# Performance work log

Hardware: AMD Instinct MI355X
Metric: run time of the kernel (lower is better)

Reference implementation:

```python
import jax, jax.numpy as jnp
import numpy as np

BLOCK = 64      # BigBird block size
HEADS = 8
N_GLOBAL = 1
WINDOW = 1      # +/-1 block sliding window
N_RAND = 3


def _build_block_idx(n_blocks, seed=0):
    """Per query block: global + window + random key blocks, causal, deduped, -1 padded."""
    rng = np.random.RandomState(seed)
    m = N_GLOBAL + (2 * WINDOW + 1) + N_RAND  # 7
    idx = np.full((n_blocks, m), -1, np.int32)
    for i in range(n_blocks):
        s = set(range(min(N_GLOBAL, i + 1)))
        for w in range(i - WINDOW, i + 1):  # causal window (blocks <= i)
            if w >= 0:
                s.add(w)
        cand = [c for c in range(i + 1) if c not in s]
        rng.shuffle(cand)
        s.update(cand[:N_RAND])
        ss = sorted(s)
        idx[i, :len(ss)] = ss
    return idx


def setup_inputs() -> dict:
    key = jax.random.key(0)
    ks = jax.random.split(key, 12)
    b, S, D = 4, 4096, 768
    dff = 4 * D
    init = lambda k, shape: (0.02 * jax.random.normal(k, shape, jnp.float32))
    return {
        'q': jax.random.normal(ks[0], (b, S, D), jnp.float32),
        'ln1_g': jnp.ones((D,), jnp.float32), 'ln1_b': jnp.zeros((D,), jnp.float32),
        'Wq': init(ks[1], (D, D)), 'bq': jnp.zeros((D,), jnp.float32),
        'Wk': init(ks[2], (D, D)), 'bk': jnp.zeros((D,), jnp.float32),
        'Wv': init(ks[3], (D, D)), 'bv': jnp.zeros((D,), jnp.float32),
        'Wo': init(ks[4], (D, D)), 'bo': jnp.zeros((D,), jnp.float32),
        'ln2_g': jnp.ones((D,), jnp.float32), 'ln2_b': jnp.zeros((D,), jnp.float32),
        'W1': init(ks[5], (D, dff)), 'b1': jnp.zeros((dff,), jnp.float32),
        'W2': init(ks[6], (dff, D)), 'b2': jnp.zeros((D,), jnp.float32),
        'key_block_idx': jnp.asarray(_build_block_idx(S // BLOCK), jnp.int32),
    }


def _layernorm(x, g, b, eps=1e-5):
    mu = jnp.mean(x, axis=-1, keepdims=True)
    var = jnp.mean(jnp.square(x - mu), axis=-1, keepdims=True)
    return (x - mu) * jax.lax.rsqrt(var + eps) * g + b


def _bigbird_attn(x, Wq, bq, Wk, bk, Wv, bv, Wo, bo, key_block_idx):
    b, S, D = x.shape
    H, hd = HEADS, D // HEADS
    nb = S // BLOCK
    m = key_block_idx.shape[1]
    proj = lambda W, bias: (x @ W + bias).reshape(b, nb, BLOCK, H, hd).transpose(0, 3, 1, 2, 4)
    q = proj(Wq, bq)  # [b,h,nb,B,hd]
    k = proj(Wk, bk)
    v = proj(Wv, bv)
    valid = key_block_idx >= 0                      # [nb, m]
    idx = jnp.maximum(key_block_idx, 0)
    kg = k[:, :, idx]                               # [b,h,nb,m,B,hd]
    vg = v[:, :, idx]
    scores = jnp.einsum('bhnqd,bhnmkd->bhnqmk', q, kg) / jnp.sqrt(jnp.float32(hd))
    off = jnp.arange(BLOCK)
    qpos = jnp.arange(nb)[:, None] * BLOCK + off    # [nb, B]
    kpos = idx[..., None] * BLOCK + off             # [nb, m, B]
    mask = valid[:, :, None] & (kpos[:, None, :, :] <= qpos[:, :, None, None])  # [nb,q,m,k]
    scores = jnp.where(mask[None, None], scores, jnp.float32(-1e9))
    attn = jax.nn.softmax(scores.reshape(b, H, nb, BLOCK, m * BLOCK), axis=-1)
    attn = attn.reshape(b, H, nb, BLOCK, m, BLOCK)
    out = jnp.einsum('bhnqmk,bhnmkd->bhnqd', attn, vg)   # [b,h,nb,B,hd]
    out = out.transpose(0, 2, 3, 1, 4).reshape(b, S, D)
    return out @ Wo + bo


def reference(q, ln1_g, ln1_b, Wq, bq, Wk, bk, Wv, bv, Wo, bo,
              ln2_g, ln2_b, W1, b1, W2, b2, key_block_idx):
    # pre-norm residual: x + attn(ln1(x))
    x = q + _bigbird_attn(_layernorm(q, ln1_g, ln1_b), Wq, bq, Wk, bk, Wv, bv, Wo, bo, key_block_idx)
    h = _layernorm(x, ln2_g, ln2_b)
    x = x + (jax.nn.gelu(h @ W1 + b1) @ W2 + b2)
    return x
```

## Files before the change

kernel.cpp:

```cpp
#include <hip/hip_runtime.h>
#include <cstdint>

typedef __bf16  bf16x8 __attribute__((ext_vector_type(8)));
typedef float   f32x4  __attribute__((ext_vector_type(4)));

__device__ __forceinline__ float bf2f(uint16_t u) {
    uint32_t x = ((uint32_t)u) << 16;
    float f; __builtin_memcpy(&f, &x, 4); return f;
}
__device__ __forceinline__ uint16_t f2bf(float f) {
    uint32_t x; __builtin_memcpy(&x, &f, 4);
    uint32_t r = (x + 0x7fffu + ((x >> 16) & 1u)) >> 16;
    return (uint16_t)r;
}
__device__ __forceinline__ float gelu_f(float x) {
    float y = 0.7978845608028654f * (x + 0.044715f * x * x * x);
    float e = __expf(-2.0f * y);
    return x * __builtin_amdgcn_rcpf(1.0f + e);
}
__device__ __forceinline__ float ldf(const void* p, size_t i, int f) {
    return f ? ((const float*)p)[i] : bf2f(((const uint16_t*)p)[i]);
}

__device__ __forceinline__ void gl_lds16(const void* g, void* lds) {
    __builtin_amdgcn_global_load_lds(
        (const __attribute__((address_space(1))) void*)g,
        (__attribute__((address_space(3))) void*)lds,
        16, 0, 0);
}

#define BATCH 4
#define SEQ   4096
#define DMODEL 768
#define HEADS 8
#define HDIM  96
#define DFF   3072
#define NBLK  64
#define MKEYS 7
#define MROWS 16384

#define SWZ(b) ((b) ^ ((((b) >> 8) & 7) << 4))

__global__ void sniff_k(const uint32_t* __restrict__ g, int* __restrict__ flag) {
    if (threadIdx.x == 0) flag[0] = (g[0] == 0x3F800000u) ? 1 : 0;
}

__global__ void transpose_k(const void* __restrict__ in, uint16_t* __restrict__ out,
                            int R, int C, const int* __restrict__ flag) {
    __shared__ float t[32][33];
    const int f = flag[0];
    int bx = blockIdx.x * 32, by = blockIdx.y * 32;
    int tx = threadIdx.x, ty = threadIdx.y;
    #pragma unroll
    for (int i = 0; i < 32; i += 8)
        t[ty + i][tx] = ldf(in, (size_t)(by + ty + i) * C + bx + tx, f);
    __syncthreads();
    #pragma unroll
    for (int i = 0; i < 32; i += 8)
        out[(size_t)(bx + ty + i) * R + by + tx] = f2bf(t[tx][ty + i]);
}

__global__ void concat_bias_k(const void* bq, const void* bk, const void* bv,
                              uint16_t* out, const int* __restrict__ flag) {
    const int f = flag[0];
    int i = blockIdx.x * 256 + threadIdx.x;
    if (i < DMODEL) {
        out[i]              = f2bf(ldf(bq, i, f));
        out[DMODEL + i]     = f2bf(ldf(bk, i, f));
        out[2 * DMODEL + i] = f2bf(ldf(bv, i, f));
    }
}

__global__ __launch_bounds__(256) void ln_k(const void* __restrict__ x,
                                            const void* __restrict__ g,
                                            const void* __restrict__ b,
                                            uint16_t* __restrict__ y,
                                            int xmode, const int* __restrict__ flag) {
    const int f = flag[0];
    const int xf = xmode ? f : 0;
    int row = blockIdx.x, tid = threadIdx.x;
    size_t base = (size_t)row * DMODEL;
    float v0 = ldf(x, base + tid, xf);
    float v1 = ldf(x, base + tid + 256, xf);
    float v2 = ldf(x, base + tid + 512, xf);
    float s = v0 + v1 + v2;
    float s2 = v0 * v0 + v1 * v1 + v2 * v2;
    #pragma unroll
    for (int off = 1; off < 64; off <<= 1) {
        s  += __shfl_xor(s, off, 64);
        s2 += __shfl_xor(s2, off, 64);
    }
    __shared__ float rs[4], rs2[4];
    if ((tid & 63) == 0) { rs[tid >> 6] = s; rs2[tid >> 6] = s2; }
    __syncthreads();
    s = rs[0] + rs[1] + rs[2] + rs[3];
    s2 = rs2[0] + rs2[1] + rs2[2] + rs2[3];
    float mu = s * (1.0f / DMODEL);
    float var = s2 * (1.0f / DMODEL) - mu * mu;
    float rstd = rsqrtf(var + 1e-5f);
    uint16_t* yr = y + base;
    yr[tid]       = f2bf((v0 - mu) * rstd * ldf(g, tid, f)       + ldf(b, tid, f));
    yr[tid + 256] = f2bf((v1 - mu) * rstd * ldf(g, tid + 256, f) + ldf(b, tid + 256, f));
    yr[tid + 512] = f2bf((v2 - mu) * rstd * ldf(g, tid + 512, f) + ldf(b, tid + 512, f));
}

template <int EPI>
__global__ __launch_bounds__(512, 2) void gemm256(
        const uint16_t* __restrict__ A, const uint16_t* __restrict__ Bt,
        const void* __restrict__ bias, const void* __restrict__ resid,
        void* __restrict__ C, int M, int N, int K,
        int bmode, int rmode, int omode, const int* __restrict__ flag) {
    __shared__ __align__(16) uint16_t SMEM[65536];
    const int f = flag[0];
    const int bf = bmode ? f : 0, rf = rmode ? f : 0, of = omode ? f : 0;
    const int tid = threadIdx.x;
    const int lane = tid & 63, wave = tid >> 6;
    const int l15 = lane & 15, quad = lane >> 4;
    const int wr = wave >> 2, wc = wave & 3;

    const int GX = gridDim.x;
    const int flat = blockIdx.y * GX + blockIdx.x;
    const int xcd = flat & 7, w8 = flat >> 3;
    const int cb = w8 % GX;
    const int rb = (w8 / GX) * 8 + xcd;
    const int m0 = rb * 256, n0 = cb * 256;
    const int NT = K >> 6;

    const uint32_t swz = ((uint32_t)((l15 >> 1) & 7)) << 4;
    const uint32_t tk0 = ((uint32_t)(quad * 16)) ^ swz;
    const uint32_t tk1 = ((uint32_t)(64 + quad * 16)) ^ swz;
    const uint32_t aA0 = (uint32_t)((wr * 64 + l15) * 128) + tk0;
    const uint32_t aA1 = (uint32_t)((wr * 64 + l15) * 128) + tk1;
    const uint32_t aB0 = 65536u + (uint32_t)((wc * 32 + l15) * 128) + tk0;
    const uint32_t aB1 = 65536u + (uint32_t)((wc * 32 + l15) * 128) + tk1;
    const char* const smb = (const char*)SMEM;

    uint32_t goff0, goff1;
    {
        uint32_t pb0 = (uint32_t)tid * 16u;
        uint32_t e0  = SWZ(pb0) >> 1;
        goff0 = (e0 >> 6) * (uint32_t)K + (e0 & 63u);
        uint32_t pb1 = (uint32_t)(512 + tid) * 16u;
        uint32_t e1  = SWZ(pb1) >> 1;
        goff1 = (e1 >> 6) * (uint32_t)K + (e1 & 63u);
    }

    f32x4 acc[2][4][2][2] = {};
    bf16x8 af[4][2], bfr[2][2][2];

    auto stage = [&](const uint16_t* __restrict__ P, int row0, int kt, uint16_t* slot) {
        const uint16_t* gb = P + (size_t)row0 * (size_t)K + (size_t)kt * 64u;
        gl_lds16(gb + goff0, slot + wave * 512);
        gl_lds16(gb + goff1, slot + 4096 + wave * 512);
    };

#define SA_(db,h)  (SMEM + ((db)*2+(h))*8192)
#define SB_(db,h)  (SMEM + 32768 + ((db)*2+(h))*8192)
#define LDA(DB,MIH) { _Pragma("unroll") for (int mi = 0; mi < 4; ++mi) {           \
      af[mi][0] = *(const bf16x8*)(smb + ((((DB)*2+(MIH))*16384) + mi*2048) + aA0);\
      af[mi][1] = *(const bf16x8*)(smb + ((((DB)*2+(MIH))*16384) + mi*2048) + aA1);} }
#define LDB(DB) { _Pragma("unroll") for (int h = 0; h < 2; ++h)                    \
      _Pragma("unroll") for (int nj = 0; nj < 2; ++nj) {                           \
      bfr[h][nj][0] = *(const bf16x8*)(smb + ((((DB)*2+h)*16384) + nj*2048) + aB0);\
      bfr[h][nj][1] = *(const bf16x8*)(smb + ((((DB)*2+h)*16384) + nj*2048) + aB1);} }
#define MM(MIH) { _Pragma("unroll") for (int ks = 0; ks < 2; ++ks)                 \
      _Pragma("unroll") for (int mi = 0; mi < 4; ++mi)                             \
      _Pragma("unroll") for (int h = 0; h < 2; ++h)                                \
      _Pragma("unroll") for (int nj = 0; nj < 2; ++nj)                             \
        acc[MIH][mi][h][nj] = __builtin_amdgcn_mfma_f32_16x16x32_bf16(             \
            af[mi][ks], bfr[h][nj][ks], acc[MIH][mi][h][nj], 0, 0, 0); }
#define BAR1  asm volatile("s_barrier" ::: "memory");                              \
              asm volatile("s_waitcnt lgkmcnt(0)" ::: "memory");                   \
              __builtin_amdgcn_sched_barrier(0)
#define PRIO1 __builtin_amdgcn_s_setprio(1)
#define PRIO0 __builtin_amdgcn_s_setprio(0); __builtin_amdgcn_sched_barrier(0)
#define BAR2  asm volatile("s_barrier" ::: "memory")

    stage(A,  m0,       0, SA_(0,0));
    stage(A,  m0 + 128, 0, SA_(0,1));
    stage(Bt, n0,       0, SB_(0,0));
    stage(Bt, n0 + 128, 0, SB_(0,1));
    stage(A,  m0,       1, SA_(1,0));
    stage(Bt, n0,       1, SB_(1,0));
    stage(Bt, n0 + 128, 1, SB_(1,1));
    asm volatile("s_waitcnt vmcnt(6)" ::: "memory");
    BAR2;

    #pragma unroll 1
    for (int tt = 0; tt < NT; tt += 2) {
        const bool last = (tt + 2 >= NT);
        LDA(0, 0); LDB(0);
        stage(A, m0 + 128, tt + 1, SA_(1,1));
        BAR1; PRIO1; MM(0); PRIO0;
        BAR2;
        LDA(0, 1);
        if (!last) { stage(A,  m0,       tt + 2, SA_(0,0));
                     stage(Bt, n0,       tt + 2, SB_(0,0));
                     stage(Bt, n0 + 128, tt + 2, SB_(0,1)); }
        BAR1; PRIO1; MM(1); PRIO0;
        if (last) { asm volatile("s_waitcnt vmcnt(2)" ::: "memory"); }
        else      { asm volatile("s_waitcnt vmcnt(8)" ::: "memory"); }
        BAR2;
        LDA(1, 0); LDB(1);
        if (!last) stage(A, m0 + 128, tt + 2, SA_(0,1));
        BAR1; PRIO1; MM(0); PRIO0;
        if (last) { asm volatile("s_waitcnt vmcnt(0)" ::: "memory"); }
        else      { asm volatile("s_waitcnt vmcnt(8)" ::: "memory"); }
        BAR2;
        LDA(1, 1);
        if (!last) { stage(A,  m0,       tt + 3, SA_(1,0));
                     stage(Bt, n0,       tt + 3, SB_(1,0));
                     stage(Bt, n0 + 128, tt + 3, SB_(1,1)); }
        BAR1; PRIO1; MM(1); PRIO0;
        if (!last) { asm volatile("s_waitcnt vmcnt(6)" ::: "memory"); }
        BAR2;
    }
#undef SA_
#undef SB_
#undef LDA
#undef LDB
#undef MM
#undef BAR1
#undef PRIO1
#undef PRIO0
#undef BAR2

    float bv[2][2];
    #pragma unroll
    for (int njh = 0; njh < 2; ++njh)
        #pragma unroll
        for (int nj = 0; nj < 2; ++nj)
            bv[njh][nj] = ldf(bias, n0 + njh * 128 + wc * 32 + nj * 16 + l15, bf);

    #pragma unroll
    for (int mih = 0; mih < 2; ++mih)
    #pragma unroll
    for (int mi = 0; mi < 4; ++mi) {
        int rowb = m0 + mih * 128 + wr * 64 + mi * 16 + quad * 4;
        #pragma unroll
        for (int njh = 0; njh < 2; ++njh)
        #pragma unroll
        for (int nj = 0; nj < 2; ++nj) {
            int col = n0 + njh * 128 + wc * 32 + nj * 16 + l15;
            #pragma unroll
            for (int r = 0; r < 4; ++r) {
                float v = acc[mih][mi][njh][nj][r] + bv[njh][nj];
                if (EPI == 2) v = gelu_f(v);
                size_t off = (size_t)(rowb + r) * N + col;
                if (EPI == 1) v += ldf(resid, off, rf);
                if (of) ((float*)C)[off] = v;
                else    ((uint16_t*)C)[off] = f2bf(v);
            }
        }
    }
}

__global__ __launch_bounds__(256) void attn_k(const __bf16* __restrict__ QKV,
                                              const int* __restrict__ kbi,
                                              uint16_t* __restrict__ Aout) {
    const int qb = blockIdx.x;
    const int h  = blockIdx.y;
    const int bb = blockIdx.z;
    const int tid = threadIdx.x;
    const int lane = tid & 63, wave = tid >> 6;
    const int l15 = lane & 15, quad = lane >> 4;

    __shared__ __align__(16) __bf16 Qs[64 * 104];
    __shared__ __align__(16) __bf16 Ks[64 * 104];
    __shared__ __align__(16) __bf16 VTs[96 * 72];
    __shared__ __align__(16) __bf16 Ps[4][16 * 72];

    const int tq = bb * SEQ + qb * 64;
    const int r0row = wave * 16 + quad * 4;
    const float sc = 0.10206207262f;

    int nv[4];
    #pragma unroll
    for (int r = 0; r < 4; ++r) {
        int cnt = 0;
        #pragma unroll
        for (int m = 0; m < MKEYS; ++m)
            cnt += (kbi[(r0row + r) * MKEYS + m] >= 0) ? 1 : 0;
        nv[r] = cnt;
    }

    for (int c = tid; c < 768; c += 256) {
        int row = c / 12, col8 = (c % 12) * 8;
        *(bf16x8*)(Qs + row * 104 + col8) =
            *(const bf16x8*)(QKV + (size_t)(tq + row) * 2304 + h * HDIM + col8);
    }

    float mrun[4] = {-1e30f, -1e30f, -1e30f, -1e30f};
    float lrun[4] = {0.f, 0.f, 0.f, 0.f};
    f32x4 oacc[6] = {};

    for (int mi = 0; mi < MKEYS; ++mi) {
        int kbraw = kbi[qb * MKEYS + mi];
        int kb = kbraw < 0 ? 0 : kbraw;
        const int tk = bb * SEQ + kb * 64;
        __syncthreads();
        for (int c = tid; c < 768; c += 256) {
            int row = c / 12, col8 = (c % 12) * 8;
            *(bf16x8*)(Ks + row * 104 + col8) =
                *(const bf16x8*)(QKV + (size_t)(tk + row) * 2304 + DMODEL + h * HDIM + col8);
        }
        for (int c = tid; c < 768; c += 256) {
            int key = c / 12, d0 = (c % 12) * 8;
            bf16x8 v = *(const bf16x8*)(QKV + (size_t)(tk + key) * 2304 + 2 * DMODEL + h * HDIM + d0);
            #pragma unroll
            for (int j2 = 0; j2 < 8; ++j2)
                VTs[(d0 + j2) * 72 + key] = v[j2];
        }
        __syncthreads();

        f32x4 s[4] = {};
        #pragma unroll
        for (int kt = 0; kt < 3; ++kt) {
            bf16x8 aq = *(const bf16x8*)(Qs + (wave * 16 + l15) * 104 + kt * 32 + quad * 8);
            #pragma unroll
            for (int j = 0; j < 4; ++j) {
                bf16x8 bk = *(const bf16x8*)(Ks + (j * 16 + l15) * 104 + kt * 32 + quad * 8);
                s[j] = __builtin_amdgcn_mfma_f32_16x16x32_bf16(aq, bk, s[j], 0, 0, 0);
            }
        }

        const bool diag = (kb == qb);
        #pragma unroll
        for (int r = 0; r < 4; ++r) {
            const bool rowen = (mi < nv[r]);
            float mx = -1e30f;
            #pragma unroll
            for (int j = 0; j < 4; ++j) {
                float v = s[j][r] * sc;
                if (!rowen || (diag && (j * 16 + l15 > r0row + r))) v = -1e30f;
                s[j][r] = v;
                mx = fmaxf(mx, v);
            }
            #pragma unroll
            for (int off = 1; off < 16; off <<= 1) mx = fmaxf(mx, __shfl_xor(mx, off, 64));
            float mnew = fmaxf(mrun[r], mx);
            float alpha = __expf(mrun[r] - mnew);
            mrun[r] = mnew;
            float ls = 0.f;
            #pragma unroll
            for (int j = 0; j < 4; ++j) {
                float p = __expf(s[j][r] - mnew);
                s[j][r] = p;
                ls += p;
            }
            #pragma unroll
            for (int off = 1; off < 16; off <<= 1) ls += __shfl_xor(ls, off, 64);
            lrun[r] = lrun[r] * alpha + ls;
            #pragma unroll
            for (int t = 0; t < 6; ++t) oacc[t][r] *= alpha;
            #pragma unroll
            for (int j = 0; j < 4; ++j)
                Ps[wave][(quad * 4 + r) * 72 + j * 16 + l15] = (__bf16)s[j][r];
        }

        __syncthreads();

        #pragma unroll
        for (int kt = 0; kt < 2; ++kt) {
            bf16x8 ap = *(const bf16x8*)(Ps[wave] + l15 * 72 + kt * 32 + quad * 8);
            #pragma unroll
            for (int t = 0; t < 6; ++t) {
                bf16x8 bv = *(const bf16x8*)(VTs + (t * 16 + l15) * 72 + kt * 32 + quad * 8);
                oacc[t] = __builtin_amdgcn_mfma_f32_16x16x32_bf16(ap, bv, oacc[t], 0, 0, 0);
            }
        }
    }

    #pragma unroll
    for (int r = 0; r < 4; ++r) {
        float inv = 1.0f / lrun[r];
        int token = tq + r0row + r;
        #pragma unroll
        for (int t = 0; t < 6; ++t) {
            int col = h * HDIM + t * 16 + l15;
            Aout[(size_t)token * DMODEL + col] = f2bf(oacc[t][r] * inv);
        }
    }
}

extern "C" void kernel_launch(void* const* d_in, const int* in_sizes, int n_in,
                              void* d_out, int out_size, void* d_ws, size_t ws_size,
                              hipStream_t stream) {
    const void* q     = d_in[0];
    const void* ln1_g = d_in[1];
    const void* ln1_b = d_in[2];
    const void* Wq    = d_in[3];
    const void* bq    = d_in[4];
    const void* Wk    = d_in[5];
    const void* bk    = d_in[6];
    const void* Wv    = d_in[7];
    const void* bv    = d_in[8];
    const void* Wo    = d_in[9];
    const void* bo    = d_in[10];
    const void* ln2_g = d_in[11];
    const void* ln2_b = d_in[12];
    const void* W1    = d_in[13];
    const void* b1    = d_in[14];
    const void* W2    = d_in[15];
    const void* b2    = d_in[16];
    const int*  kbi   = (const int*)d_in[17];
    char* ws = (char*)d_ws;

    uint16_t* WqkvT = (uint16_t*)(ws + 0);
    uint16_t* WoT   = (uint16_t*)(ws + 3538944);
    uint16_t* W1T   = (uint16_t*)(ws + 4718592);
    uint16_t* W2T   = (uint16_t*)(ws + 9437184);
    uint16_t* bqkv  = (uint16_t*)(ws + 14155776);
    int*      flag  = (int*)(ws + 14160384);
    uint16_t* x1    = (uint16_t*)(ws + 14160896);
    uint16_t* QKV   = (uint16_t*)(ws + 39326720);
    uint16_t* attn  = (uint16_t*)(ws + 114824192);
    uint16_t* xb    = (uint16_t*)(ws + 139990016);
    uint16_t* mid   = QKV;

    sniff_k<<<1, 64, 0, stream>>>((const uint32_t*)ln1_g, flag);

    dim3 tb(32, 8);
    transpose_k<<<dim3(24, 24), tb, 0, stream>>>(Wq, WqkvT, DMODEL, DMODEL, flag);
    transpose_k<<<dim3(24, 24), tb, 0, stream>>>(Wk, WqkvT + DMODEL * DMODEL, DMODEL, DMODEL, flag);
    transpose_k<<<dim3(24, 24), tb, 0, stream>>>(Wv, WqkvT + 2 * DMODEL * DMODEL, DMODEL, DMODEL, flag);
    transpose_k<<<dim3(24, 24), tb, 0, stream>>>(Wo, WoT, DMODEL, DMODEL, flag);
    transpose_k<<<dim3(96, 24), tb, 0, stream>>>(W1, W1T, DMODEL, DFF, flag);
    transpose_k<<<dim3(24, 96), tb, 0, stream>>>(W2, W2T, DFF, DMODEL, flag);
    concat_bias_k<<<3, 256, 0, stream>>>(bq, bk, bv, bqkv, flag);

    ln_k<<<MROWS, 256, 0, stream>>>(q, ln1_g, ln1_b, x1, 1, flag);
    gemm256<0><<<dim3(9, 64), 512, 0, stream>>>(x1, WqkvT, bqkv, nullptr, QKV,
                                                MROWS, 3 * DMODEL, DMODEL, 0, 0, 0, flag);
    attn_k<<<dim3(NBLK, HEADS, BATCH), 256, 0, stream>>>((const __bf16*)QKV, kbi, attn);
    gemm256<1><<<dim3(3, 64), 512, 0, stream>>>(attn, WoT, bo, q, xb,
                                                MROWS, DMODEL, DMODEL, 1, 1, 0, flag);
    ln_k<<<MROWS, 256, 0, stream>>>(xb, ln2_g, ln2_b, x1, 0, flag);
    gemm256<2><<<dim3(12, 64), 512, 0, stream>>>(x1, W1T, b1, nullptr, mid,
                                                 MROWS, DFF, DMODEL, 1, 0, 0, flag);
    gemm256<1><<<dim3(3, 64), 512, 0, stream>>>(mid, W2T, b2, xb, d_out,
                                                MROWS, DMODEL, DFF, 1, 0, 1, flag);
}
```

Baseline: 694.0 us.

## Prefetch next K/V tile into registers, keep Q in registers, swizzle LDS

```diff
diff --git a/kernel.cpp b/kernel.cpp
--- a/kernel.cpp
+++ b/kernel.cpp
@@ -255,20 +255,24 @@
     }
 }
 
-__global__ __launch_bounds__(256) void attn_k(const __bf16* __restrict__ QKV,
-                                              const int* __restrict__ kbi,
-                                              uint16_t* __restrict__ Aout) {
+__global__ __launch_bounds__(256, 4) void attn_k(const __bf16* __restrict__ QKV,
+                                                 const int* __restrict__ kbi,
+                                                 uint16_t* __restrict__ Aout) {
     const int qb = blockIdx.x;
     const int h  = blockIdx.y;
     const int bb = blockIdx.z;
     const int tid = threadIdx.x;
     const int lane = tid & 63, wave = tid >> 6;
     const int l15 = lane & 15, quad = lane >> 4;
-
-    __shared__ __align__(16) __bf16 Qs[64 * 104];
-    __shared__ __align__(16) __bf16 Ks[64 * 104];
+    const int h8 = l15 >> 3;
+
+    __shared__ __align__(16) __bf16 Ks[64 * 96];
     __shared__ __align__(16) __bf16 VTs[96 * 72];
-    __shared__ __align__(16) __bf16 Ps[4][16 * 72];
+    __shared__ __align__(16) __bf16 Ps[4 * 16 * 72];
+
+    char* const ksb = (char*)Ks;
+    char* const vtb = (char*)VTs;
+    char* const psb = (char*)Ps + wave * 2304;
 
     const int tq = bb * SEQ + qb * 64;
     const int r0row = wave * 16 + quad * 4;
@@ -284,47 +288,78 @@
         nv[r] = cnt;
     }
 
-    for (int c = tid; c < 768; c += 256) {
-        int row = c / 12, col8 = (c % 12) * 8;
-        *(bf16x8*)(Qs + row * 104 + col8) =
-            *(const bf16x8*)(QKV + (size_t)(tq + row) * 2304 + h * HDIM + col8);
-    }
+    bf16x8 aq[3];
+    {
+        const __bf16* qp = QKV + (size_t)(tq + wave * 16 + l15) * 2304 + h * HDIM + quad * 8;
+        aq[0] = *(const bf16x8*)(qp);
+        aq[1] = *(const bf16x8*)(qp + 32);
+        aq[2] = *(const bf16x8*)(qp + 64);
+    }
+
+    uint32_t goff[3], kwb[3], vtw[3];
+    #pragma unroll
+    for (int i = 0; i < 3; ++i) {
+        int c = i * 256 + tid;
+        int r = c / 12, cm = c % 12;
+        goff[i] = (uint32_t)(r * 2304 + cm * 8);
+        kwb[i]  = (uint32_t)(r * 192 + ((cm ^ (r & 3)) << 4));
+        vtw[i]  = (uint32_t)(cm * 8 * 144 + ((r * 2) ^ ((cm & 7) << 4)));
+    }
+
+    bf16x8 kreg[3], vreg[3];
+    auto load_tile = [&](int kb) {
+        const __bf16* base = QKV + (size_t)(bb * SEQ + kb * 64) * 2304 + h * HDIM;
+        #pragma unroll
+        for (int i = 0; i < 3; ++i) {
+            kreg[i] = *(const bf16x8*)(base + DMODEL + goff[i]);
+            vreg[i] = *(const bf16x8*)(base + 2 * DMODEL + goff[i]);
+        }
+    };
+    auto write_tile = [&]() {
+        #pragma unroll
+        for (int i = 0; i < 3; ++i) {
+            *(bf16x8*)(ksb + kwb[i]) = kreg[i];
+            #pragma unroll
+            for (int j2 = 0; j2 < 8; ++j2)
+                *(__bf16*)(vtb + vtw[i] + j2 * 144) = vreg[i][j2];
+        }
+    };
+
+    int kb0 = kbi[qb * MKEYS + 0];
+    int kb_cur = kb0 < 0 ? 0 : kb0;
+    load_tile(kb_cur);
+    write_tile();
+    __syncthreads();
 
     float mrun[4] = {-1e30f, -1e30f, -1e30f, -1e30f};
     float lrun[4] = {0.f, 0.f, 0.f, 0.f};
     f32x4 oacc[6] = {};
 
+    const uint32_t kq16 = (uint32_t)((quad ^ (l15 & 3)) << 4);
+    const uint32_t prB  = (uint32_t)((quad << 4) ^ ((l15 >> 2) << 4));
+    const uint32_t vq   = (uint32_t)(((quad ^ h8) << 4));
+
     for (int mi = 0; mi < MKEYS; ++mi) {
-        int kbraw = kbi[qb * MKEYS + mi];
-        int kb = kbraw < 0 ? 0 : kbraw;
-        const int tk = bb * SEQ + kb * 64;
-        __syncthreads();
-        for (int c = tid; c < 768; c += 256) {
-            int row = c / 12, col8 = (c % 12) * 8;
-            *(bf16x8*)(Ks + row * 104 + col8) =
-                *(const bf16x8*)(QKV + (size_t)(tk + row) * 2304 + DMODEL + h * HDIM + col8);
-        }
-        for (int c = tid; c < 768; c += 256) {
-            int key = c / 12, d0 = (c % 12) * 8;
-            bf16x8 v = *(const bf16x8*)(QKV + (size_t)(tk + key) * 2304 + 2 * DMODEL + h * HDIM + d0);
-            #pragma unroll
-            for (int j2 = 0; j2 < 8; ++j2)
-                VTs[(d0 + j2) * 72 + key] = v[j2];
-        }
-        __syncthreads();
+        int kb_nxt = 0;
+        if (mi + 1 < MKEYS) {
+            kb_nxt = kbi[qb * MKEYS + mi + 1];
+            kb_nxt = kb_nxt < 0 ? 0 : kb_nxt;
+            load_tile(kb_nxt);
+        }
 
         f32x4 s[4] = {};
+        __builtin_amdgcn_s_setprio(1);
         #pragma unroll
         for (int kt = 0; kt < 3; ++kt) {
-            bf16x8 aq = *(const bf16x8*)(Qs + (wave * 16 + l15) * 104 + kt * 32 + quad * 8);
             #pragma unroll
             for (int j = 0; j < 4; ++j) {
-                bf16x8 bk = *(const bf16x8*)(Ks + (j * 16 + l15) * 104 + kt * 32 + quad * 8);
-                s[j] = __builtin_amdgcn_mfma_f32_16x16x32_bf16(aq, bk, s[j], 0, 0, 0);
+                bf16x8 bk = *(const bf16x8*)(ksb + (j * 16 + l15) * 192 + kt * 64 + kq16);
+                s[j] = __builtin_amdgcn_mfma_f32_16x16x32_bf16(aq[kt], bk, s[j], 0, 0, 0);
             }
         }
-
-        const bool diag = (kb == qb);
+        __builtin_amdgcn_s_setprio(0);
+
+        const bool diag = (kb_cur == qb);
         #pragma unroll
         for (int r = 0; r < 4; ++r) {
             const bool rowen = (mi < nv[r]);
@@ -355,19 +390,33 @@
             for (int t = 0; t < 6; ++t) oacc[t][r] *= alpha;
             #pragma unroll
             for (int j = 0; j < 4; ++j)
-                Ps[wave][(quad * 4 + r) * 72 + j * 16 + l15] = (__bf16)s[j][r];
-        }
-
-        __syncthreads();
-
+                *(__bf16*)(psb + (quad * 4 + r) * 144 +
+                           (((uint32_t)(j * 32) | (uint32_t)(l15 * 2)) ^ ((uint32_t)quad << 4)))
+                    = (__bf16)s[j][r];
+        }
+
+        asm volatile("s_waitcnt lgkmcnt(0)" ::: "memory");
+        __builtin_amdgcn_sched_barrier(0);
+
+        __builtin_amdgcn_s_setprio(1);
         #pragma unroll
         for (int kt = 0; kt < 2; ++kt) {
-            bf16x8 ap = *(const bf16x8*)(Ps[wave] + l15 * 72 + kt * 32 + quad * 8);
+            bf16x8 ap = *(const bf16x8*)(psb + l15 * 144 + kt * 64 + prB);
             #pragma unroll
             for (int t = 0; t < 6; ++t) {
-                bf16x8 bv = *(const bf16x8*)(VTs + (t * 16 + l15) * 72 + kt * 32 + quad * 8);
+                const uint32_t L = (uint32_t)((((2 * t) & 7) << 4) ^ (kt << 6));
+                bf16x8 bv = *(const bf16x8*)(vtb + (t * 16 + l15) * 144 +
+                                             ((uint32_t)(quad << 4) ^ (uint32_t)(h8 << 4) ^ L));
                 oacc[t] = __builtin_amdgcn_mfma_f32_16x16x32_bf16(ap, bv, oacc[t], 0, 0, 0);
             }
+        }
+        __builtin_amdgcn_s_setprio(0);
+
+        if (mi + 1 < MKEYS) {
+            __syncthreads();
+            write_tile();
+            __syncthreads();
+            kb_cur = kb_nxt;
         }
     }
 
```

After: 634.2 us. -8.6%, faster.
